# Kernel optimization log

Measured on AMD Instinct MI355X. Metric: run time of the kernel, lower is better.

Reference implementation:

```python
import jax, jax.numpy as jnp
import numpy as np


def setup_inputs() -> dict:
    key = jax.random.key(0)
    k1, k2, k3 = jax.random.split(key, 3)
    B, N1, N2 = 2, 8192, 8192
    xyz1 = jax.random.normal(k1, (B, 3, N1), dtype=jnp.float32)
    xyz2 = jax.random.normal(k2, (B, 3, N2), dtype=jnp.float32)
    flow1 = 0.1 * jax.random.normal(k3, (B, 3, N1), dtype=jnp.float32)
    return {"xyz1": xyz1, "xyz2": xyz2, "flow1": flow1, "K": 16}


def reference(xyz1, xyz2, flow1, K):
    # PointWarping3 with initial_radius == 0 (KNN branch).
    # xyz1, xyz2, flow1: [B, 3, N]
    p1 = (xyz1 + flow1).transpose(0, 2, 1)   # xyz1_to_2, [B, N1, 3]
    p2 = xyz2.transpose(0, 2, 1)             # [B, N2, 3]
    f1 = flow1.transpose(0, 2, 1)            # [B, N1, 3]
    # pairwise squared distances [B, N2, N1]
    d2 = ((p2 * p2).sum(-1, keepdims=True)
          - 2.0 * jnp.einsum('bnc,bmc->bnm', p2, p1)
          + (p1 * p1).sum(-1)[:, None, :])
    _, idx = jax.lax.top_k(-d2, K)           # K nearest source points, [B, N2, K]
    grouped = jax.vmap(lambda f, i: f[i])(f1, idx)  # gather flows, [B, N2, K, 3]
    flow2 = grouped.mean(axis=2)             # [B, N2, 3]
    warped_xyz2 = (p2 - flow2).transpose(0, 2, 1)   # [B, 3, N2]
    return warped_xyz2
```

## Files before the change

### kernel.cpp

```cpp
#include <hip/hip_runtime.h>
#include <math.h>

#define N1 8192
#define N2 8192
#define NBATCH 2
#define KNN 16
#define NBUCKET 512
#define BWF 0.015625f
#define XMINF (-4.0f)
#define NCHUNKS 128

typedef unsigned int uint;
typedef unsigned long long ull;

__global__ __launch_bounds__(256) void pw3_prep(
    const float* __restrict__ xyz1, const float* __restrict__ flow1,
    uint* __restrict__ hist) {
  int i = blockIdx.x * 256 + threadIdx.x;
  int b = i >> 13, m = i & (N1 - 1);
  float px = xyz1[b * 3 * N1 + m] + flow1[b * 3 * N1 + m];
  int bk = (int)floorf((px - XMINF) * (1.0f / BWF));
  bk = min(max(bk, 0), NBUCKET - 1);
  atomicAdd(&hist[(b << 9) + bk], 1u);
}

__global__ __launch_bounds__(1024) void pw3_scan(
    const uint* __restrict__ hist, uint* __restrict__ offs,
    uint* __restrict__ cur) {
  __shared__ uint buf[1024];
  int t = threadIdx.x;
  int i = t & (NBUCKET - 1);
  uint h = hist[t];
  buf[t] = h;
  __syncthreads();
  for (int off = 1; off < NBUCKET; off <<= 1) {
    uint a = (i >= off) ? buf[t - off] : 0u;
    __syncthreads();
    buf[t] += a;
    __syncthreads();
  }
  uint ex = buf[t] - h;
  offs[t] = ex;
  cur[t] = ex;
}

__global__ __launch_bounds__(256) void pw3_scatter(
    const float* __restrict__ xyz1, const float* __restrict__ flow1,
    uint* __restrict__ cur, float4* __restrict__ sp4,
    uint* __restrict__ minb, uint* __restrict__ maxb) {
  int i = blockIdx.x * 256 + threadIdx.x;
  int b = i >> 13, m = i & (N1 - 1);
  const float* x1 = xyz1 + b * 3 * N1;
  const float* f1 = flow1 + b * 3 * N1;
  float px = x1[m] + f1[m];
  float py = x1[N1 + m] + f1[N1 + m];
  float pz = x1[2 * N1 + m] + f1[2 * N1 + m];
  int bk = (int)floorf((px - XMINF) * (1.0f / BWF));
  bk = min(max(bk, 0), NBUCKET - 1);
  uint pos = atomicAdd(&cur[(b << 9) + bk], 1u);
  float4 v;
  v.x = px; v.y = py; v.z = pz; v.w = __int_as_float(m);
  sp4[(b << 13) + pos] = v;
  int c = (int)(pos >> 6);
  atomicMin(&minb[(b << 7) + c], (uint)bk);
  atomicMax(&maxb[(b << 7) + c], (uint)bk);
}

__device__ __forceinline__ float dpp_up1_f(float x, float old_v) {
  int r = __builtin_amdgcn_update_dpp(
      __builtin_bit_cast(int, old_v), __builtin_bit_cast(int, x),
      0x111, 0xf, 0xf, false);
  return __builtin_bit_cast(float, r);
}
__device__ __forceinline__ int dpp_up1_i(int x) {
  return __builtin_amdgcn_update_dpp(0, x, 0x111, 0xf, 0xf, false);
}
template <int J>
__device__ __forceinline__ int lx_i(int x) {
  if constexpr (J == 1)
    return __builtin_amdgcn_update_dpp(x, x, 0xB1, 0xf, 0xf, false);
  else if constexpr (J == 2)
    return __builtin_amdgcn_update_dpp(x, x, 0x4E, 0xf, 0xf, false);
  else if constexpr (J == 32)
    return __shfl_xor(x, 32);
  else
    return __builtin_amdgcn_ds_swizzle(x, (J << 10) | 0x1F);
}
template <int J>
__device__ __forceinline__ float lx_f(float x) {
  return __builtin_bit_cast(float, lx_i<J>(__builtin_bit_cast(int, x)));
}

__global__ __launch_bounds__(256) void pw3_knn(
    const float* __restrict__ xyz2, const float4* __restrict__ sp4,
    const float* __restrict__ flow1, const uint* __restrict__ offs,
    const uint* __restrict__ minb, const uint* __restrict__ maxb,
    float* __restrict__ out) {
  int lane = threadIdx.x & 63;
  int sub = lane & 15;
  int wid = (int)((blockIdx.x * 256 + threadIdx.x) >> 6);
  int b = wid >> 13;
  int n = wid & (N2 - 1);

  const float* x2 = xyz2 + b * 3 * N2;
  float qx = x2[n], qy = x2[N2 + n], qz = x2[2 * N2 + n];
  float n2 = (qx * qx + qy * qy) + qz * qz;

  const float4* __restrict__ src = sp4 + ((size_t)b << 13);

  int mb0 = (int)minb[(b << 7) + lane];
  int mb1 = (int)minb[(b << 7) + 64 + lane];
  int xb0 = (int)maxb[(b << 7) + lane];
  int xb1 = (int)maxb[(b << 7) + 64 + lane];

  int bq = min(max((int)floorf((qx - XMINF) * (1.0f / BWF)), 0), NBUCKET - 1);
  uint off0 = offs[(b << 9) + bq];
  int cs = min((int)(off0 >> 6), NCHUNKS - 1);

  float4 s = src[cs * 64 + lane];
  float dv;
  int iv = __float_as_int(s.w);
  {
    float nn = fmaf(s.z, s.z, fmaf(s.y, s.y, s.x * s.x));
    float dot = fmaf(s.z, qz, fmaf(s.y, qy, s.x * qx));
    dv = (n2 - 2.0f * dot) + nn;
  }
#define CE64(K, Jv)                                                  \
  {                                                                  \
    float pd = lx_f<Jv>(dv);                                         \
    int pi = lx_i<Jv>(iv);                                           \
    bool ms = (dv < pd) || ((dv == pd) && (iv < pi));                \
    bool km = ((lane & (K)) == 0) == ((lane & (Jv)) == 0);           \
    bool tm = (ms == km);                                            \
    dv = tm ? dv : pd;                                               \
    iv = tm ? iv : pi;                                               \
  }
  CE64(2, 1)
  CE64(4, 2) CE64(4, 1)
  CE64(8, 4) CE64(8, 2) CE64(8, 1)
  CE64(16, 8) CE64(16, 4) CE64(16, 2) CE64(16, 1)
  CE64(32, 16) CE64(32, 8) CE64(32, 4) CE64(32, 2) CE64(32, 1)
  CE64(64, 32) CE64(64, 16) CE64(64, 8) CE64(64, 4) CE64(64, 2) CE64(64, 1)
#undef CE64

  float val = __shfl(dv, sub);
  int vidx = __shfl(iv, sub);
  float kth = __builtin_bit_cast(
      float, __builtin_amdgcn_readlane(__builtin_bit_cast(int, val), 15));

  const float NEG_INF = -INFINITY, INF = INFINITY;
  int lc = cs - 1, rc = cs + 1;

  auto rd128 = [&](int r0, int r1, int c) -> int {
    int a = __builtin_amdgcn_readlane(r0, c & 63);
    int bb = __builtin_amdgcn_readlane(r1, c & 63);
    return (c & 64) ? bb : a;
  };
  auto decide = [&]() -> int {
    float lg = INF, rg = INF;
    if (lc >= 0) {
      int mv = rd128(xb0, xb1, lc);
      float hi = (mv >= NBUCKET - 1) ? INF : (XMINF + (mv + 1) * BWF);
      lg = fmaxf(qx - hi, 0.0f);
    }
    if (rc <= NCHUNKS - 1) {
      int mv = rd128(mb0, mb1, rc);
      float lo = (mv <= 0) ? -INF : (XMINF + mv * BWF);
      rg = fmaxf(lo - qx, 0.0f);
    }
    bool left = lg <= rg;
    float g = left ? lg : rg;
    if (!(g * g <= kth)) return -1;
    int c = left ? lc : rc;
    if (left) --lc; else ++rc;
    return c;
  };

  int c0 = decide();
  float4 s0v;
  if (c0 >= 0) s0v = src[c0 * 64 + lane];
  while (c0 >= 0) {
    int c1 = decide();
    float4 s1v;
    if (c1 >= 0) s1v = src[c1 * 64 + lane];

    int civ = __float_as_int(s0v.w);
    float nn = fmaf(s0v.z, s0v.z, fmaf(s0v.y, s0v.y, s0v.x * s0v.x));
    float dot = fmaf(s0v.z, qz, fmaf(s0v.y, qy, s0v.x * qx));
    float d = (n2 - 2.0f * dot) + nn;

    ull bal = __ballot(d < kth);
    if (bal) {
      int dbits = __builtin_bit_cast(int, d);
      do {
        int l = __ffsll(bal) - 1;
        bal &= bal - 1;
        float cd = __builtin_bit_cast(
            float, __builtin_amdgcn_readlane(dbits, l));
        int ci = __builtin_amdgcn_readlane(civ, l);
        float pv = dpp_up1_f(val, NEG_INF);
        int pi = dpp_up1_i(vidx);
        bool lt = cd < val;
        bool ltp = cd < pv;
        val = lt ? (ltp ? pv : cd) : val;
        vidx = lt ? (ltp ? pi : ci) : vidx;
      } while (bal);
      kth = __builtin_bit_cast(
          float, __builtin_amdgcn_readlane(__builtin_bit_cast(int, val), 15));
    }
    c0 = c1;
    s0v = s1v;
  }

  const float* f1 = flow1 + b * 3 * N1;
  float fx = f1[vidx], fy = f1[N1 + vidx], fz = f1[2 * N1 + vidx];
  #pragma unroll
  for (int o = 8; o > 0; o >>= 1) {
    fx += __shfl_xor(fx, o);
    fy += __shfl_xor(fy, o);
    fz += __shfl_xor(fz, o);
  }

  if (lane == 0) {
    float* op = out + b * 3 * N2;
    const float inv_k = 1.0f / KNN;
    op[n]          = qx - fx * inv_k;
    op[N2 + n]     = qy - fy * inv_k;
    op[2 * N2 + n] = qz - fz * inv_k;
  }
}

extern "C" void kernel_launch(void* const* d_in, const int* in_sizes, int n_in,
                              void* d_out, int out_size, void* d_ws, size_t ws_size,
                              hipStream_t stream) {
  const float* xyz1  = (const float*)d_in[0];
  const float* xyz2  = (const float*)d_in[1];
  const float* flow1 = (const float*)d_in[2];
  float* out = (float*)d_out;

  char* w = (char*)d_ws;
  float4* sp4 = (float4*)w;            w += (size_t)NBATCH * N1 * sizeof(float4);
  uint* offs  = (uint*)w;              w += NBATCH * NBUCKET * sizeof(uint);
  uint* cur   = (uint*)w;              w += NBATCH * NBUCKET * sizeof(uint);
  uint* minb  = (uint*)w;              w += NBATCH * NCHUNKS * sizeof(uint);
  uint* hist  = (uint*)w;              w += NBATCH * NBUCKET * sizeof(uint);
  uint* maxb  = (uint*)w;              w += NBATCH * NCHUNKS * sizeof(uint);

  hipMemsetAsync(minb, 0xFF, NBATCH * NCHUNKS * sizeof(uint), stream);
  hipMemsetAsync(hist, 0,
                 NBATCH * NBUCKET * sizeof(uint) + NBATCH * NCHUNKS * sizeof(uint),
                 stream);

  pw3_prep<<<(NBATCH * N1) / 256, 256, 0, stream>>>(xyz1, flow1, hist);
  pw3_scan<<<1, 1024, 0, stream>>>(hist, offs, cur);
  pw3_scatter<<<(NBATCH * N1) / 256, 256, 0, stream>>>(xyz1, flow1, cur, sp4,
                                                       minb, maxb);
  pw3_knn<<<(NBATCH * N2 * 64) / 256, 256, 0, stream>>>(xyz2, sp4, flow1, offs,
                                                        minb, maxb, out);
}
```

Measured before the change: 120.2 us.

## Fuse binning into one block per batch and batch-merge KNN candidates

Replaces the prep, scan and scatter kernels plus two memsets with a single pw3_build kernel per batch that builds the histogram, scan and scatter in shared memory and emits float chunk bounds. The KNN kernel now seeds its top-16 from four neighbouring chunks using a 64-wide bitonic merge, and falls back to that merge instead of serial insertion when many lanes qualify. It also precomputes chunk x-bounds as floats and adds a small epsilon to the pruning test. The aim is to cut launch overhead and serial readlane loops. The cost is a build phase run by only two blocks and extra merge work per query.

New measurement: 97.54 us. 1.23x faster.

```diff
diff --git a/kernel.cpp b/kernel.cpp
--- a/kernel.cpp
+++ b/kernel.cpp
@@ -9,61 +9,74 @@
 #define BWF 0.015625f
 #define XMINF (-4.0f)
 #define NCHUNKS 128
+#define SER_MAX 12
 
 typedef unsigned int uint;
 typedef unsigned long long ull;
 
-__global__ __launch_bounds__(256) void pw3_prep(
+__global__ __launch_bounds__(1024) void pw3_build(
     const float* __restrict__ xyz1, const float* __restrict__ flow1,
-    uint* __restrict__ hist) {
-  int i = blockIdx.x * 256 + threadIdx.x;
-  int b = i >> 13, m = i & (N1 - 1);
-  float px = xyz1[b * 3 * N1 + m] + flow1[b * 3 * N1 + m];
-  int bk = (int)floorf((px - XMINF) * (1.0f / BWF));
-  bk = min(max(bk, 0), NBUCKET - 1);
-  atomicAdd(&hist[(b << 9) + bk], 1u);
-}
-
-__global__ __launch_bounds__(1024) void pw3_scan(
-    const uint* __restrict__ hist, uint* __restrict__ offs,
-    uint* __restrict__ cur) {
-  __shared__ uint buf[1024];
+    float4* __restrict__ sp4, uint* __restrict__ offs,
+    float* __restrict__ lox, float* __restrict__ hix) {
+  __shared__ uint hist[NBUCKET];
+  __shared__ uint scn[NBUCKET];
+  __shared__ uint cmin[NCHUNKS];
+  __shared__ uint cmax[NCHUNKS];
+  int b = blockIdx.x;
   int t = threadIdx.x;
-  int i = t & (NBUCKET - 1);
-  uint h = hist[t];
-  buf[t] = h;
-  __syncthreads();
-  for (int off = 1; off < NBUCKET; off <<= 1) {
-    uint a = (i >= off) ? buf[t - off] : 0u;
-    __syncthreads();
-    buf[t] += a;
-    __syncthreads();
-  }
-  uint ex = buf[t] - h;
-  offs[t] = ex;
-  cur[t] = ex;
-}
-
-__global__ __launch_bounds__(256) void pw3_scatter(
-    const float* __restrict__ xyz1, const float* __restrict__ flow1,
-    uint* __restrict__ cur, float4* __restrict__ sp4,
-    uint* __restrict__ minb, uint* __restrict__ maxb) {
-  int i = blockIdx.x * 256 + threadIdx.x;
-  int b = i >> 13, m = i & (N1 - 1);
+  if (t < NBUCKET) hist[t] = 0u;
+  if (t < NCHUNKS) { cmin[t] = 0xFFFFFFFFu; cmax[t] = 0u; }
+  __syncthreads();
   const float* x1 = xyz1 + b * 3 * N1;
   const float* f1 = flow1 + b * 3 * N1;
-  float px = x1[m] + f1[m];
-  float py = x1[N1 + m] + f1[N1 + m];
-  float pz = x1[2 * N1 + m] + f1[2 * N1 + m];
-  int bk = (int)floorf((px - XMINF) * (1.0f / BWF));
-  bk = min(max(bk, 0), NBUCKET - 1);
-  uint pos = atomicAdd(&cur[(b << 9) + bk], 1u);
-  float4 v;
-  v.x = px; v.y = py; v.z = pz; v.w = __int_as_float(m);
-  sp4[(b << 13) + pos] = v;
-  int c = (int)(pos >> 6);
-  atomicMin(&minb[(b << 7) + c], (uint)bk);
-  atomicMax(&maxb[(b << 7) + c], (uint)bk);
+  float px[8], py[8], pz[8];
+  int bk[8];
+  #pragma unroll
+  for (int r = 0; r < 8; ++r) {
+    int m = r * 1024 + t;
+    px[r] = x1[m] + f1[m];
+    py[r] = x1[N1 + m] + f1[N1 + m];
+    pz[r] = x1[2 * N1 + m] + f1[2 * N1 + m];
+    int bb = (int)floorf((px[r] - XMINF) * (1.0f / BWF));
+    bk[r] = min(max(bb, 0), NBUCKET - 1);
+    atomicAdd(&hist[bk[r]], 1u);
+  }
+  __syncthreads();
+  uint h = 0;
+  if (t < NBUCKET) { h = hist[t]; scn[t] = h; }
+  __syncthreads();
+  for (int off = 1; off < NBUCKET; off <<= 1) {
+    uint v = 0;
+    if (t < NBUCKET && t >= off) v = scn[t - off];
+    __syncthreads();
+    if (t < NBUCKET) scn[t] += v;
+    __syncthreads();
+  }
+  if (t < NBUCKET) {
+    uint ex = scn[t] - h;
+    offs[(b << 9) + t] = ex;
+    hist[t] = ex;
+  }
+  __syncthreads();
+  #pragma unroll
+  for (int r = 0; r < 8; ++r) {
+    int m = r * 1024 + t;
+    uint pos = atomicAdd(&hist[bk[r]], 1u);
+    float4 v;
+    v.x = px[r]; v.y = py[r]; v.z = pz[r]; v.w = __int_as_float(m);
+    sp4[(b << 13) + pos] = v;
+    int c = (int)(pos >> 6);
+    atomicMin(&cmin[c], (uint)bk[r]);
+    atomicMax(&cmax[c], (uint)bk[r]);
+  }
+  __syncthreads();
+  if (t < NCHUNKS) {
+    float lo = (cmin[t] == 0u) ? -INFINITY : (XMINF + (float)cmin[t] * BWF);
+    float hi = (cmax[t] >= (uint)(NBUCKET - 1)) ? INFINITY
+                                                : (XMINF + (float)(cmax[t] + 1u) * BWF);
+    lox[(b << 7) + t] = lo;
+    hix[(b << 7) + t] = hi;
+  }
 }
 
 __device__ __forceinline__ float dpp_up1_f(float x, float old_v) {
@@ -81,20 +94,63 @@
     return __builtin_amdgcn_update_dpp(x, x, 0xB1, 0xf, 0xf, false);
   else if constexpr (J == 2)
     return __builtin_amdgcn_update_dpp(x, x, 0x4E, 0xf, 0xf, false);
-  else if constexpr (J == 32)
-    return __shfl_xor(x, 32);
+  else if constexpr (J <= 31)
+    return __builtin_amdgcn_ds_swizzle(x, (J << 10) | 0x1F);
   else
-    return __builtin_amdgcn_ds_swizzle(x, (J << 10) | 0x1F);
+    return __shfl_xor(x, J);
 }
 template <int J>
 __device__ __forceinline__ float lx_f(float x) {
   return __builtin_bit_cast(float, lx_i<J>(__builtin_bit_cast(int, x)));
 }
+__device__ __forceinline__ float rl_f(float v, int l) {
+  return __builtin_bit_cast(
+      float, __builtin_amdgcn_readlane(__builtin_bit_cast(int, v), l));
+}
+
+__device__ __forceinline__ void merge64(float cd, int ci, int sub,
+                                        float& val, int& vidx) {
+#define CEP(vd, vi, J, KM)                                           \
+  {                                                                  \
+    float pd_ = lx_f<J>(vd);                                         \
+    int pi_ = lx_i<J>(vi);                                           \
+    bool ms_ = (vd < pd_) || ((vd == pd_) && (vi < pi_));            \
+    bool tm_ = (ms_ == ((((KM) >> sub) & 1) != 0));                  \
+    vd = tm_ ? vd : pd_;                                             \
+    vi = tm_ ? vi : pi_;                                             \
+  }
+  CEP(cd, ci, 1, 0x9999u) CEP(cd, ci, 2, 0xC3C3u) CEP(cd, ci, 1, 0xA5A5u)
+  CEP(cd, ci, 4, 0xF00Fu) CEP(cd, ci, 2, 0xCC33u) CEP(cd, ci, 1, 0xAA55u)
+  CEP(cd, ci, 8, 0x00FFu) CEP(cd, ci, 4, 0x0F0Fu) CEP(cd, ci, 2, 0x3333u)
+  CEP(cd, ci, 1, 0x5555u)
+  {
+    float pd = lx_f<31>(cd); int pi = lx_i<31>(ci);
+    bool ms = (cd < pd) || ((cd == pd) && (ci < pi));
+    cd = ms ? cd : pd; ci = ms ? ci : pi;
+  }
+  CEP(cd, ci, 8, 0x00FFu) CEP(cd, ci, 4, 0x0F0Fu) CEP(cd, ci, 2, 0x3333u)
+  CEP(cd, ci, 1, 0x5555u)
+  {
+    float pd = lx_f<47>(cd); int pi = lx_i<47>(ci);
+    bool ms = (cd < pd) || ((cd == pd) && (ci < pi));
+    cd = ms ? cd : pd; ci = ms ? ci : pi;
+  }
+  CEP(cd, ci, 8, 0x00FFu) CEP(cd, ci, 4, 0x0F0Fu) CEP(cd, ci, 2, 0x3333u)
+  CEP(cd, ci, 1, 0x5555u)
+  {
+    float pd = lx_f<15>(val); int pi = lx_i<15>(vidx);
+    bool ms = (cd < pd) || ((cd == pd) && (ci < pi));
+    val = ms ? cd : pd; vidx = ms ? ci : pi;
+  }
+  CEP(val, vidx, 8, 0x00FFu) CEP(val, vidx, 4, 0x0F0Fu)
+  CEP(val, vidx, 2, 0x3333u) CEP(val, vidx, 1, 0x5555u)
+#undef CEP
+}
 
 __global__ __launch_bounds__(256) void pw3_knn(
     const float* __restrict__ xyz2, const float4* __restrict__ sp4,
     const float* __restrict__ flow1, const uint* __restrict__ offs,
-    const uint* __restrict__ minb, const uint* __restrict__ maxb,
+    const float* __restrict__ lox, const float* __restrict__ hix,
     float* __restrict__ out) {
   int lane = threadIdx.x & 63;
   int sub = lane & 15;
@@ -108,22 +164,22 @@
 
   const float4* __restrict__ src = sp4 + ((size_t)b << 13);
 
-  int mb0 = (int)minb[(b << 7) + lane];
-  int mb1 = (int)minb[(b << 7) + 64 + lane];
-  int xb0 = (int)maxb[(b << 7) + lane];
-  int xb1 = (int)maxb[(b << 7) + 64 + lane];
+  float hx0 = hix[(b << 7) + lane];
+  float hx1 = hix[(b << 7) + 64 + lane];
+  float lo0 = lox[(b << 7) + lane];
+  float lo1 = lox[(b << 7) + 64 + lane];
 
   int bq = min(max((int)floorf((qx - XMINF) * (1.0f / BWF)), 0), NBUCKET - 1);
-  uint off0 = offs[(b << 9) + bq];
-  int cs = min((int)(off0 >> 6), NCHUNKS - 1);
-
-  float4 s = src[cs * 64 + lane];
-  float dv;
-  int iv = __float_as_int(s.w);
+  int cs = min((int)(offs[(b << 9) + bq] >> 6), NCHUNKS - 1);
+  int cs0 = min(max(cs - 1, 0), NCHUNKS - 4);
+
+  float dv; int iv;
   {
+    float4 s = src[cs * 64 + lane];
     float nn = fmaf(s.z, s.z, fmaf(s.y, s.y, s.x * s.x));
     float dot = fmaf(s.z, qz, fmaf(s.y, qy, s.x * qx));
     dv = (n2 - 2.0f * dot) + nn;
+    iv = __float_as_int(s.w);
   }
 #define CE64(K, Jv)                                                  \
   {                                                                  \
@@ -145,32 +201,35 @@
 
   float val = __shfl(dv, sub);
   int vidx = __shfl(iv, sub);
-  float kth = __builtin_bit_cast(
-      float, __builtin_amdgcn_readlane(__builtin_bit_cast(int, val), 15));
-
-  const float NEG_INF = -INFINITY, INF = INFINITY;
-  int lc = cs - 1, rc = cs + 1;
-
-  auto rd128 = [&](int r0, int r1, int c) -> int {
-    int a = __builtin_amdgcn_readlane(r0, c & 63);
-    int bb = __builtin_amdgcn_readlane(r1, c & 63);
-    return (c & 64) ? bb : a;
+
+  #pragma unroll
+  for (int j = 0; j < 4; ++j) {
+    int cj = cs0 + j;
+    if (cj != cs) {
+      float4 s = src[cj * 64 + lane];
+      float nn = fmaf(s.z, s.z, fmaf(s.y, s.y, s.x * s.x));
+      float dot = fmaf(s.z, qz, fmaf(s.y, qy, s.x * qx));
+      float dd = (n2 - 2.0f * dot) + nn;
+      merge64(dd, __float_as_int(s.w), sub, val, vidx);
+    }
+  }
+  float kth = rl_f(val, 15);
+
+  const float NEG_INF = -INFINITY;
+  int lc = cs0 - 1, rc = cs0 + 4;
+
+  auto rd128f = [&](float r0, float r1, int c) -> float {
+    int a = __builtin_amdgcn_readlane(__builtin_bit_cast(int, r0), c & 63);
+    int bb = __builtin_amdgcn_readlane(__builtin_bit_cast(int, r1), c & 63);
+    return __builtin_bit_cast(float, (c & 64) ? bb : a);
   };
   auto decide = [&]() -> int {
-    float lg = INF, rg = INF;
-    if (lc >= 0) {
-      int mv = rd128(xb0, xb1, lc);
-      float hi = (mv >= NBUCKET - 1) ? INF : (XMINF + (mv + 1) * BWF);
-      lg = fmaxf(qx - hi, 0.0f);
-    }
-    if (rc <= NCHUNKS - 1) {
-      int mv = rd128(mb0, mb1, rc);
-      float lo = (mv <= 0) ? -INF : (XMINF + mv * BWF);
-      rg = fmaxf(lo - qx, 0.0f);
-    }
+    float lg = INFINITY, rg = INFINITY;
+    if (lc >= 0)       lg = fmaxf(qx - rd128f(hx0, hx1, lc), 0.0f);
+    if (rc < NCHUNKS)  rg = fmaxf(rd128f(lo0, lo1, rc) - qx, 0.0f);
     bool left = lg <= rg;
     float g = left ? lg : rg;
-    if (!(g * g <= kth)) return -1;
+    if (!(g * g <= kth + 1e-6f)) return -1;
     int c = left ? lc : rc;
     if (left) --lc; else ++rc;
     return c;
@@ -191,22 +250,26 @@
 
     ull bal = __ballot(d < kth);
     if (bal) {
-      int dbits = __builtin_bit_cast(int, d);
-      do {
-        int l = __ffsll(bal) - 1;
-        bal &= bal - 1;
-        float cd = __builtin_bit_cast(
-            float, __builtin_amdgcn_readlane(dbits, l));
-        int ci = __builtin_amdgcn_readlane(civ, l);
-        float pv = dpp_up1_f(val, NEG_INF);
-        int pi = dpp_up1_i(vidx);
-        bool lt = cd < val;
-        bool ltp = cd < pv;
-        val = lt ? (ltp ? pv : cd) : val;
-        vidx = lt ? (ltp ? pi : ci) : vidx;
-      } while (bal);
-      kth = __builtin_bit_cast(
-          float, __builtin_amdgcn_readlane(__builtin_bit_cast(int, val), 15));
+      int cnt = (int)__popcll(bal);
+      if (cnt <= SER_MAX) {
+        int dbits = __builtin_bit_cast(int, d);
+        do {
+          int l = __ffsll(bal) - 1;
+          bal &= bal - 1;
+          float cd = __builtin_bit_cast(
+              float, __builtin_amdgcn_readlane(dbits, l));
+          int ci2 = __builtin_amdgcn_readlane(civ, l);
+          float pv = dpp_up1_f(val, NEG_INF);
+          int pi = dpp_up1_i(vidx);
+          bool lt = cd < val;
+          bool ltp = cd < pv;
+          val = lt ? (ltp ? pv : cd) : val;
+          vidx = lt ? (ltp ? pi : ci2) : vidx;
+        } while (bal);
+      } else {
+        merge64(d, civ, sub, val, vidx);
+      }
+      kth = rl_f(val, 15);
     }
     c0 = c1;
     s0v = s1v;
@@ -239,22 +302,12 @@
   float* out = (float*)d_out;
 
   char* w = (char*)d_ws;
-  float4* sp4 = (float4*)w;            w += (size_t)NBATCH * N1 * sizeof(float4);
-  uint* offs  = (uint*)w;              w += NBATCH * NBUCKET * sizeof(uint);
-  uint* cur   = (uint*)w;              w += NBATCH * NBUCKET * sizeof(uint);
-  uint* minb  = (uint*)w;              w += NBATCH * NCHUNKS * sizeof(uint);
-  uint* hist  = (uint*)w;              w += NBATCH * NBUCKET * sizeof(uint);
-  uint* maxb  = (uint*)w;              w += NBATCH * NCHUNKS * sizeof(uint);
-
-  hipMemsetAsync(minb, 0xFF, NBATCH * NCHUNKS * sizeof(uint), stream);
-  hipMemsetAsync(hist, 0,
-                 NBATCH * NBUCKET * sizeof(uint) + NBATCH * NCHUNKS * sizeof(uint),
-                 stream);
-
-  pw3_prep<<<(NBATCH * N1) / 256, 256, 0, stream>>>(xyz1, flow1, hist);
-  pw3_scan<<<1, 1024, 0, stream>>>(hist, offs, cur);
-  pw3_scatter<<<(NBATCH * N1) / 256, 256, 0, stream>>>(xyz1, flow1, cur, sp4,
-                                                       minb, maxb);
+  float4* sp4 = (float4*)w;  w += (size_t)NBATCH * N1 * sizeof(float4);
+  uint* offs  = (uint*)w;    w += NBATCH * NBUCKET * sizeof(uint);
+  float* lox  = (float*)w;   w += NBATCH * NCHUNKS * sizeof(float);
+  float* hix  = (float*)w;   w += NBATCH * NCHUNKS * sizeof(float);
+
+  pw3_build<<<NBATCH, 1024, 0, stream>>>(xyz1, flow1, sp4, offs, lox, hix);
   pw3_knn<<<(NBATCH * N2 * 64) / 256, 256, 0, stream>>>(xyz2, sp4, flow1, offs,
-                                                        minb, maxb, out);
-}
+                                                        lox, hix, out);
+}
```
